# Kernel tuning notes

Hardware: AMD Instinct MI355X
Metric: run time of the kernel (lower is better)

The kernel has to match this reference:

```python
import jax, jax.numpy as jnp
import numpy as np

B, N, IN_F = 8, 1024, 512
H, D = 4, 128  # num_heads, out_features; H*D == IN_F for residual
LN_EPS = 1e-5
NEG_INF = -1e9


def setup_inputs() -> dict:
    key = jax.random.key(0)
    ks = jax.random.split(key, 7)
    x = jax.random.normal(ks[0], (B, N, IN_F), dtype=jnp.float32)
    mask = jax.random.randint(ks[1], (B, N), 0, 2, dtype=jnp.int32)
    # xavier-uniform-ish init scales
    W = jax.random.uniform(ks[2], (IN_F, H * D), dtype=jnp.float32, minval=-1.0, maxval=1.0) * (1.414 * np.sqrt(6.0 / (IN_F + H * D)))
    a_src = jax.random.uniform(ks[3], (H, D), dtype=jnp.float32, minval=-1.0, maxval=1.0) * (1.414 * np.sqrt(6.0 / (H + D)))
    a_dst = jax.random.uniform(ks[4], (H, D), dtype=jnp.float32, minval=-1.0, maxval=1.0) * (1.414 * np.sqrt(6.0 / (H + D)))
    gamma = jnp.ones((H * D,), dtype=jnp.float32)
    beta = jnp.zeros((H * D,), dtype=jnp.float32)
    return {"x": x, "mask": mask, "W": W, "a_src": a_src, "a_dst": a_dst, "gamma": gamma, "beta": beta}


def _layernorm(y, gamma, beta):
    mu = jnp.mean(y, axis=-1, keepdims=True)
    var = jnp.var(y, axis=-1, keepdims=True)
    return (y - mu) * jax.lax.rsqrt(var + LN_EPS) * gamma + beta


def reference(x, mask, W, a_src, a_dst, gamma, beta):
    b, n, _ = x.shape
    h = (x @ W).reshape(b, n, H, D)                      # [B,N,H,D]
    e_i = jnp.einsum('bnhd,hd->bnh', h, a_src)           # [B,N,H]
    e_j = jnp.einsum('bnhd,hd->bnh', h, a_dst)           # [B,N,H]
    e = jax.nn.leaky_relu(e_i[:, :, None, :] + e_j[:, None, :, :], 0.2)  # [B,N,N,H]
    mm = mask[:, None, :, None] * mask[:, :, None, None]  # [B,N,N,1]
    e = jnp.where(mm == 0, NEG_INF, e)
    attn = jax.nn.softmax(e, axis=2)                     # softmax over neighbors j
    h_prime = jnp.einsum('bnjh,bjhd->bnhd', attn, h).reshape(b, n, H * D)
    return _layernorm(h_prime + x, gamma, beta)
```

## Files before the change

kernel.cpp:

```cpp
#include <hip/hip_runtime.h>
#include <math.h>

#define Bsz 8
#define Nn 1024
#define Ff 512
#define Hh 4
#define Dd 128

typedef float f32x4 __attribute__((ext_vector_type(4)));
typedef short bf16x8 __attribute__((ext_vector_type(8)));

__device__ inline uint f2b1(float a) {
    union { float f; uint u; } v; v.f = a;
    return (v.u + 0x7fffu + ((v.u >> 16) & 1u)) >> 16;
}
__device__ inline uint f2b_pk(float a, float b) { return f2b1(a) | (f2b1(b) << 16); }


__global__ __launch_bounds__(256) void conv_xw(const float* __restrict__ X,
                                               const float* __restrict__ Wm,
                                               ushort* __restrict__ Xc,
                                               ushort* __restrict__ Wc) {
    __shared__ float tile[8 * 520];
    const int bi = blockIdx.x, tid = threadIdx.x;
    if (bi < 512) {
        const int mtile = (bi & 7) * 64 + (bi >> 3);
        const int kblk = tid >> 2, m15b = (tid & 3) * 4;
        #pragma unroll
        for (int c = 0; c < 4; ++c) {
            int m15 = m15b + c;
            const float4* xp = (const float4*)(X + (size_t)(mtile * 16 + m15) * Ff + kblk * 8);
            float4 f0 = xp[0], f1 = xp[1];
            uint4 o = { f2b_pk(f0.x, f0.y), f2b_pk(f0.z, f0.w),
                        f2b_pk(f1.x, f1.y), f2b_pk(f1.z, f1.w) };
            *(uint4*)(Xc + (((size_t)(mtile * 64 + kblk) * 16 + m15) << 3)) = o;
        }
    } else {
        const int kb = bi - 512;
        const int l = tid & 63, wv = tid >> 6;
        const int col0 = l * 8;
        #pragma unroll
        for (int rsel = 0; rsel < 2; ++rsel) {
            int kr = wv + rsel * 4;
            const float4* wp = (const float4*)(Wm + (size_t)(kb * 8 + kr) * Ff + col0);
            float4 a = wp[0], c = wp[1];
            *(float4*)(&tile[kr * 520 + col0]) = a;
            *(float4*)(&tile[kr * 520 + col0 + 4]) = c;
        }
        __syncthreads();
        #pragma unroll
        for (int rsel = 0; rsel < 2; ++rsel) {
            int n = tid + rsel * 256;
            float v[8];
            #pragma unroll
            for (int u = 0; u < 8; ++u) v[u] = tile[u * 520 + n];
            uint4 o = { f2b_pk(v[0], v[1]), f2b_pk(v[2], v[3]),
                        f2b_pk(v[4], v[5]), f2b_pk(v[6], v[7]) };
            int nc = n >> 7, nt = (n >> 4) & 7, n15 = n & 15;
            *(uint4*)(Wc + ((size_t)(((nc * 64 + kb) * 8 + nt) * 16 + n15) << 3)) = o;
        }
    }
}

__global__ __launch_bounds__(256, 2) void gemm_xw(const ushort* __restrict__ Xc,
                                                  const ushort* __restrict__ Wc,
                                                  const float* __restrict__ a_src,
                                                  const float* __restrict__ a_dst,
                                                  ushort* __restrict__ hT,
                                                  float* __restrict__ ei,
                                                  float* __restrict__ ej) {
    const int idx = blockIdx.x;
    const int b = idx & 7, sub = idx >> 3;
    const int mi = sub & 15, nc = sub >> 4;
    const int tid = threadIdx.x;
    const int w = tid >> 6, lane = tid & 63, quad = lane >> 4, l16 = lane & 15;
    const int mtile = (b * 16 + mi) * 4 + w;

    f32x4 z = {0.f, 0.f, 0.f, 0.f};
    f32x4 acc[8];
    #pragma unroll
    for (int nt = 0; nt < 8; ++nt) acc[nt] = z;

    const ushort* ap = Xc + ((size_t)mtile << 13) + quad * 128 + l16 * 8;
    const ushort* bp = Wc + ((size_t)nc << 16) + quad * 1024 + l16 * 8;

    bf16x8 ab[2];
    bf16x8 bb[2][8];
    ab[0] = *(const bf16x8*)(ap);
    ab[1] = *(const bf16x8*)(ap + 512);
    #pragma unroll
    for (int nt = 0; nt < 8; ++nt) {
        bb[0][nt] = *(const bf16x8*)(bp + nt * 128);
        bb[1][nt] = *(const bf16x8*)(bp + 4096 + nt * 128);
    }

    #pragma unroll 2
    for (int s = 0; s < 16; ++s) {
        const int c = s & 1;
        #pragma unroll
        for (int nt = 0; nt < 8; ++nt)
            acc[nt] = __builtin_amdgcn_mfma_f32_16x16x32_bf16(ab[c], bb[c][nt], acc[nt], 0, 0, 0);
        if (s + 2 < 16) {
            ab[c] = *(const bf16x8*)(ap + (s + 2) * 512);
            #pragma unroll
            for (int nt = 0; nt < 8; ++nt)
                bb[c][nt] = *(const bf16x8*)(bp + (s + 2) * 4096 + nt * 128);
        }
    }

    const int nseq = (mi * 4 + w) * 16 + quad * 4;
    const int jb = nseq >> 5, js = nseq & 31;
    #pragma unroll
    for (int nt = 0; nt < 8; ++nt) {
        uint2 pv;
        pv.x = f2b_pk(acc[nt][0], acc[nt][1]);
        pv.y = f2b_pk(acc[nt][2], acc[nt][3]);
        int hd = nc * 128 + nt * 16 + l16;
        *(uint2*)(hT + ((size_t)(b * 32 + jb)) * 16384 + (size_t)hd * 32 + js) = pv;
    }

    {
        float as4[8], ad4[8];
        #pragma unroll
        for (int nt = 0; nt < 8; ++nt) {
            as4[nt] = a_src[nc * 128 + nt * 16 + l16];
            ad4[nt] = a_dst[nc * 128 + nt * 16 + l16];
        }
        #pragma unroll
        for (int rr = 0; rr < 4; ++rr) {
            float v1 = 0.f, v2 = 0.f;
            #pragma unroll
            for (int nt = 0; nt < 8; ++nt) {
                v1 += acc[nt][rr] * as4[nt];
                v2 += acc[nt][rr] * ad4[nt];
            }
            #pragma unroll
            for (int off = 1; off < 16; off <<= 1) {
                v1 += __shfl_xor(v1, off);
                v2 += __shfl_xor(v2, off);
            }
            if (l16 == 0) {
                int n = nseq + rr;
                ei[((b * 4 + nc) << 10) + n] = v1;
                ej[((b * 4 + nc) << 10) + n] = v2;
            }
        }
    }
}

__global__ __launch_bounds__(512, 2) void attn_pv(const ushort* __restrict__ hT,
                                                  const float* __restrict__ ei_g,
                                                  const float* __restrict__ ej_g,
                                                  const int* __restrict__ mask,
                                                  const float* __restrict__ X,
                                                  const float* __restrict__ gamma,
                                                  const float* __restrict__ beta,
                                                  float* __restrict__ out) {
    __shared__ float s_ep[32 * 516];
    __shared__ float s_as[4][32];

    const int idx = blockIdx.x;
    const int b = idx & 7, i0 = (idx >> 3) * 32;
    const int tid = threadIdx.x;
    const int w = tid >> 6, w4 = w & 3, jh = w >> 2;
    const int lane = tid & 63, quad = lane >> 4, l16 = lane & 15;

    const float* ejh = ej_g + ((b * 4 + w4) << 10);
    const int* mkb = mask + (b << 10);

    float maxej = -3.0e38f;
    #pragma unroll
    for (int k = 0; k < 16; ++k) maxej = fmaxf(maxej, ejh[lane + 64 * k]);
    #pragma unroll
    for (int off = 1; off < 64; off <<= 1) maxej = fmaxf(maxej, __shfl_xor(maxej, off));

    const float ei0 = ei_g[((b * 4 + w4) << 10) + i0 + l16];
    const float ei1 = ei_g[((b * 4 + w4) << 10) + i0 + 16 + l16];
    const int mi0 = mkb[i0 + l16];
    const int mi1 = mkb[i0 + 16 + l16];
    float m0, m1;
    { float t = ei0 + maxej; m0 = mi0 ? fmaxf(t, 0.2f * t) : -1e9f; }
    { float t = ei1 + maxej; m1 = mi1 ? fmaxf(t, 0.2f * t) : -1e9f; }

    f32x4 z = {0.f, 0.f, 0.f, 0.f};
    f32x4 acc[2][8], asum[2];
    #pragma unroll
    for (int it = 0; it < 2; ++it) { asum[it] = z;
        #pragma unroll
        for (int dt = 0; dt < 8; ++dt) acc[it][dt] = z; }
    bf16x8 ones;
    #pragma unroll
    for (int q = 0; q < 8; ++q) ones[q] = (short)0x3F80;

    const ushort* hTb = hT + ((size_t)(b * 32)) * 16384 + (size_t)(w4 * 128) * 32
                        + l16 * 32 + quad * 8;

    bf16x8 B[2][8];
    #pragma unroll
    for (int c = 0; c < 2; ++c) {
        const ushort* h0 = hTb + (size_t)(jh * 16 + c) * 16384;
        #pragma unroll
        for (int dt = 0; dt < 8; ++dt) B[c][dt] = *(const bf16x8*)(h0 + dt * 512);
    }

    #pragma unroll 2
    for (int r = 0; r < 16; ++r) {
        const int c = r & 1;
        const int jq = (jh * 16 + r) * 32 + quad * 8;
        float4 e0 = *(const float4*)(ejh + jq);
        float4 e1 = *(const float4*)(ejh + jq + 4);
        int4 q0 = *(const int4*)(mkb + jq);
        int4 q1 = *(const int4*)(mkb + jq + 4);
        float ev[8] = {e0.x, e0.y, e0.z, e0.w, e1.x, e1.y, e1.z, e1.w};
        int   mv[8] = {q0.x, q0.y, q0.z, q0.w, q1.x, q1.y, q1.z, q1.w};
        float wv0[8], wv1[8];
        #pragma unroll
        for (int u = 0; u < 8; ++u) {
            float t0 = ei0 + ev[u];
            float l0 = fmaxf(t0, 0.2f * t0);
            wv0[u] = __expf(((mi0 && mv[u]) ? l0 : -1e9f) - m0);
            float t1 = ei1 + ev[u];
            float l1 = fmaxf(t1, 0.2f * t1);
            wv1[u] = __expf(((mi1 && mv[u]) ? l1 : -1e9f) - m1);
        }
        union { uint4 u; bf16x8 v; } af0, af1;
        af0.u.x = f2b_pk(wv0[0], wv0[1]); af0.u.y = f2b_pk(wv0[2], wv0[3]);
        af0.u.z = f2b_pk(wv0[4], wv0[5]); af0.u.w = f2b_pk(wv0[6], wv0[7]);
        af1.u.x = f2b_pk(wv1[0], wv1[1]); af1.u.y = f2b_pk(wv1[2], wv1[3]);
        af1.u.z = f2b_pk(wv1[4], wv1[5]); af1.u.w = f2b_pk(wv1[6], wv1[7]);
        asum[0] = __builtin_amdgcn_mfma_f32_16x16x32_bf16(af0.v, ones, asum[0], 0, 0, 0);
        asum[1] = __builtin_amdgcn_mfma_f32_16x16x32_bf16(af1.v, ones, asum[1], 0, 0, 0);
        #pragma unroll
        for (int dt = 0; dt < 8; ++dt) {
            acc[0][dt] = __builtin_amdgcn_mfma_f32_16x16x32_bf16(af0.v, B[c][dt], acc[0][dt], 0, 0, 0);
            acc[1][dt] = __builtin_amdgcn_mfma_f32_16x16x32_bf16(af1.v, B[c][dt], acc[1][dt], 0, 0, 0);
        }
        if (r + 2 < 16) {
            const ushort* hn = hTb + (size_t)(jh * 16 + r + 2) * 16384;
            #pragma unroll
            for (int dt = 0; dt < 8; ++dt) B[c][dt] = *(const bf16x8*)(hn + dt * 512);
        }
    }

    if (jh == 1) {
        #pragma unroll
        for (int it = 0; it < 2; ++it)
            #pragma unroll
            for (int dt = 0; dt < 8; ++dt)
                #pragma unroll
                for (int rr = 0; rr < 4; ++rr)
                    s_ep[(it * 16 + quad * 4 + rr) * 516 + w4 * 128 + dt * 16 + l16] =
                        acc[it][dt][rr];
        if (l16 == 0) {
            #pragma unroll
            for (int it = 0; it < 2; ++it)
                #pragma unroll
                for (int rr = 0; rr < 4; ++rr)
                    s_as[w4][it * 16 + quad * 4 + rr] = asum[it][rr];
        }
    }
    __syncthreads();
    if (jh == 0) {
        float rs[2][4];
        #pragma unroll
        for (int it = 0; it < 2; ++it)
            #pragma unroll
            for (int rr = 0; rr < 4; ++rr)
                rs[it][rr] = 1.f / (asum[it][rr] + s_as[w4][it * 16 + quad * 4 + rr]);
        #pragma unroll
        for (int it = 0; it < 2; ++it)
            #pragma unroll
            for (int dt = 0; dt < 8; ++dt)
                #pragma unroll
                for (int rr = 0; rr < 4; ++rr) {
                    int off = (it * 16 + quad * 4 + rr) * 516 + w4 * 128 + dt * 16 + l16;
                    s_ep[off] = (acc[it][dt][rr] + s_ep[off]) * rs[it][rr];
                }
    }
    __syncthreads();

    #pragma unroll
    for (int q = 0; q < 4; ++q) {
        int ir = w * 4 + q;
        int ig = i0 + ir;
        float4 p0 = *(const float4*)(&s_ep[ir * 516 + lane * 8]);
        float4 p1 = *(const float4*)(&s_ep[ir * 516 + lane * 8 + 4]);
        const float* xp = X + (((size_t)((b << 10) + ig)) << 9) + lane * 8;
        float4 x0 = *(const float4*)(xp);
        float4 x1 = *(const float4*)(xp + 4);
        float v[8] = {p0.x + x0.x, p0.y + x0.y, p0.z + x0.z, p0.w + x0.w,
                      p1.x + x1.x, p1.y + x1.y, p1.z + x1.z, p1.w + x1.w};
        float s1 = 0.f, s2 = 0.f;
        #pragma unroll
        for (int u = 0; u < 8; ++u) { s1 += v[u]; s2 += v[u] * v[u]; }
        #pragma unroll
        for (int off = 1; off < 64; off <<= 1) { s1 += __shfl_xor(s1, off); s2 += __shfl_xor(s2, off); }
        float mean = s1 * (1.f / 512.f);
        float var  = s2 * (1.f / 512.f) - mean * mean;
        float rstd = rsqrtf(var + 1e-5f);
        int f0i = lane * 8;
        float4 g0 = *(const float4*)(gamma + f0i);
        float4 g1 = *(const float4*)(gamma + f0i + 4);
        float4 be0 = *(const float4*)(beta + f0i);
        float4 be1 = *(const float4*)(beta + f0i + 4);
        float* op = out + (((size_t)((b << 10) + ig)) << 9) + f0i;
        float4 o0, o1;
        o0.x = (v[0] - mean) * rstd * g0.x + be0.x;
        o0.y = (v[1] - mean) * rstd * g0.y + be0.y;
        o0.z = (v[2] - mean) * rstd * g0.z + be0.z;
        o0.w = (v[3] - mean) * rstd * g0.w + be0.w;
        o1.x = (v[4] - mean) * rstd * g1.x + be1.x;
        o1.y = (v[5] - mean) * rstd * g1.y + be1.y;
        o1.z = (v[6] - mean) * rstd * g1.z + be1.z;
        o1.w = (v[7] - mean) * rstd * g1.w + be1.w;
        *(float4*)op = o0;
        *(float4*)(op + 4) = o1;
    }
}

extern "C" void kernel_launch(void* const* d_in, const int* in_sizes, int n_in,
                              void* d_out, int out_size, void* d_ws, size_t ws_size,
                              hipStream_t stream) {
    const float* x     = (const float*)d_in[0];
    const int*   mask  = (const int*)d_in[1];
    const float* W     = (const float*)d_in[2];
    const float* a_src = (const float*)d_in[3];
    const float* a_dst = (const float*)d_in[4];
    const float* gamma = (const float*)d_in[5];
    const float* beta  = (const float*)d_in[6];
    float* out = (float*)d_out;

    ushort* hT = (ushort*)d_ws;
    ushort* Xc = hT + (size_t)8 * 512 * 1024;
    ushort* Wc = Xc + (size_t)8 * 1024 * 512;
    float* ei = (float*)(Wc + (size_t)512 * 512);
    float* ej = ei + 32768;

    conv_xw<<<dim3(576), 256, 0, stream>>>(x, W, Xc, Wc);
    gemm_xw<<<dim3(512), 256, 0, stream>>>(Xc, Wc, a_src, a_dst, hT, ei, ej);
    attn_pv<<<dim3(256), 512, 0, stream>>>(hT, ei, ej, mask, x, gamma, beta, out);
}
```

Before: 126.2 us.

## Fuse X bf16 conversion into GEMM loads and use exp2 with log2e-scaled logits

Removes the separate pass that converted X to a tiled bf16 buffer. The GEMM now reads fp32 X directly and converts it to bf16 in registers, which saves a full write and re-read of X through global memory. The attention logits are pre-scaled by log2(e) so the softmax can call the hardware exp2 instruction instead of __expf. The trade-off is that the GEMM A-operand loads become strided fp32 row reads of twice the size, which may be less coalesced than the old pre-tiled layout.

```diff
diff --git a/kernel.cpp b/kernel.cpp
--- a/kernel.cpp
+++ b/kernel.cpp
@@ -10,6 +10,8 @@
 typedef float f32x4 __attribute__((ext_vector_type(4)));
 typedef short bf16x8 __attribute__((ext_vector_type(8)));
 
+#define LOG2E 1.44269504f
+
 __device__ inline uint f2b1(float a) {
     union { float f; uint u; } v; v.f = a;
     return (v.u + 0x7fffu + ((v.u >> 16) & 1u)) >> 16;
@@ -17,52 +19,35 @@
 __device__ inline uint f2b_pk(float a, float b) { return f2b1(a) | (f2b1(b) << 16); }
 
 
-__global__ __launch_bounds__(256) void conv_xw(const float* __restrict__ X,
-                                               const float* __restrict__ Wm,
-                                               ushort* __restrict__ Xc,
-                                               ushort* __restrict__ Wc) {
+__global__ __launch_bounds__(256) void conv_w(const float* __restrict__ Wm,
+                                              ushort* __restrict__ Wc) {
     __shared__ float tile[8 * 520];
-    const int bi = blockIdx.x, tid = threadIdx.x;
-    if (bi < 512) {
-        const int mtile = (bi & 7) * 64 + (bi >> 3);
-        const int kblk = tid >> 2, m15b = (tid & 3) * 4;
-        #pragma unroll
-        for (int c = 0; c < 4; ++c) {
-            int m15 = m15b + c;
-            const float4* xp = (const float4*)(X + (size_t)(mtile * 16 + m15) * Ff + kblk * 8);
-            float4 f0 = xp[0], f1 = xp[1];
-            uint4 o = { f2b_pk(f0.x, f0.y), f2b_pk(f0.z, f0.w),
-                        f2b_pk(f1.x, f1.y), f2b_pk(f1.z, f1.w) };
-            *(uint4*)(Xc + (((size_t)(mtile * 64 + kblk) * 16 + m15) << 3)) = o;
-        }
-    } else {
-        const int kb = bi - 512;
-        const int l = tid & 63, wv = tid >> 6;
-        const int col0 = l * 8;
-        #pragma unroll
-        for (int rsel = 0; rsel < 2; ++rsel) {
-            int kr = wv + rsel * 4;
-            const float4* wp = (const float4*)(Wm + (size_t)(kb * 8 + kr) * Ff + col0);
-            float4 a = wp[0], c = wp[1];
-            *(float4*)(&tile[kr * 520 + col0]) = a;
-            *(float4*)(&tile[kr * 520 + col0 + 4]) = c;
-        }
-        __syncthreads();
-        #pragma unroll
-        for (int rsel = 0; rsel < 2; ++rsel) {
-            int n = tid + rsel * 256;
-            float v[8];
-            #pragma unroll
-            for (int u = 0; u < 8; ++u) v[u] = tile[u * 520 + n];
-            uint4 o = { f2b_pk(v[0], v[1]), f2b_pk(v[2], v[3]),
-                        f2b_pk(v[4], v[5]), f2b_pk(v[6], v[7]) };
-            int nc = n >> 7, nt = (n >> 4) & 7, n15 = n & 15;
-            *(uint4*)(Wc + ((size_t)(((nc * 64 + kb) * 8 + nt) * 16 + n15) << 3)) = o;
-        }
-    }
-}
-
-__global__ __launch_bounds__(256, 2) void gemm_xw(const ushort* __restrict__ Xc,
+    const int kb = blockIdx.x, tid = threadIdx.x;
+    const int l = tid & 63, wv = tid >> 6;
+    const int col0 = l * 8;
+    #pragma unroll
+    for (int rsel = 0; rsel < 2; ++rsel) {
+        int kr = wv + rsel * 4;
+        const float4* wp = (const float4*)(Wm + (size_t)(kb * 8 + kr) * Ff + col0);
+        float4 a = wp[0], c = wp[1];
+        *(float4*)(&tile[kr * 520 + col0]) = a;
+        *(float4*)(&tile[kr * 520 + col0 + 4]) = c;
+    }
+    __syncthreads();
+    #pragma unroll
+    for (int rsel = 0; rsel < 2; ++rsel) {
+        int n = tid + rsel * 256;
+        float v[8];
+        #pragma unroll
+        for (int u = 0; u < 8; ++u) v[u] = tile[u * 520 + n];
+        uint4 o = { f2b_pk(v[0], v[1]), f2b_pk(v[2], v[3]),
+                    f2b_pk(v[4], v[5]), f2b_pk(v[6], v[7]) };
+        int nc = n >> 7, nt = (n >> 4) & 7, n15 = n & 15;
+        *(uint4*)(Wc + ((size_t)(((nc * 64 + kb) * 8 + nt) * 16 + n15) << 3)) = o;
+    }
+}
+
+__global__ __launch_bounds__(256, 2) void gemm_xw(const float* __restrict__ X,
                                                   const ushort* __restrict__ Wc,
                                                   const float* __restrict__ a_src,
                                                   const float* __restrict__ a_dst,
@@ -81,13 +66,21 @@
     #pragma unroll
     for (int nt = 0; nt < 8; ++nt) acc[nt] = z;
 
-    const ushort* ap = Xc + ((size_t)mtile << 13) + quad * 128 + l16 * 8;
+    const float* ap = X + (size_t)(mtile * 16 + l16) * Ff + quad * 8;
     const ushort* bp = Wc + ((size_t)nc << 16) + quad * 1024 + l16 * 8;
+
+#define LOADA(s, dst) { \
+        float4 f0_ = *(const float4*)(ap + (s) * 32); \
+        float4 f1_ = *(const float4*)(ap + (s) * 32 + 4); \
+        union { uint4 u; bf16x8 v; } o_; \
+        o_.u.x = f2b_pk(f0_.x, f0_.y); o_.u.y = f2b_pk(f0_.z, f0_.w); \
+        o_.u.z = f2b_pk(f1_.x, f1_.y); o_.u.w = f2b_pk(f1_.z, f1_.w); \
+        dst = o_.v; }
 
     bf16x8 ab[2];
     bf16x8 bb[2][8];
-    ab[0] = *(const bf16x8*)(ap);
-    ab[1] = *(const bf16x8*)(ap + 512);
+    LOADA(0, ab[0]);
+    LOADA(1, ab[1]);
     #pragma unroll
     for (int nt = 0; nt < 8; ++nt) {
         bb[0][nt] = *(const bf16x8*)(bp + nt * 128);
@@ -101,12 +94,13 @@
         for (int nt = 0; nt < 8; ++nt)
             acc[nt] = __builtin_amdgcn_mfma_f32_16x16x32_bf16(ab[c], bb[c][nt], acc[nt], 0, 0, 0);
         if (s + 2 < 16) {
-            ab[c] = *(const bf16x8*)(ap + (s + 2) * 512);
+            LOADA(s + 2, ab[c]);
             #pragma unroll
             for (int nt = 0; nt < 8; ++nt)
                 bb[c][nt] = *(const bf16x8*)(bp + (s + 2) * 4096 + nt * 128);
         }
     }
+#undef LOADA
 
     const int nseq = (mi * 4 + w) * 16 + quad * 4;
     const int jb = nseq >> 5, js = nseq & 31;
@@ -123,8 +117,8 @@
         float as4[8], ad4[8];
         #pragma unroll
         for (int nt = 0; nt < 8; ++nt) {
-            as4[nt] = a_src[nc * 128 + nt * 16 + l16];
-            ad4[nt] = a_dst[nc * 128 + nt * 16 + l16];
+            as4[nt] = a_src[nc * 128 + nt * 16 + l16] * LOG2E;
+            ad4[nt] = a_dst[nc * 128 + nt * 16 + l16] * LOG2E;
         }
         #pragma unroll
         for (int rr = 0; rr < 4; ++rr) {
@@ -218,10 +212,10 @@
         for (int u = 0; u < 8; ++u) {
             float t0 = ei0 + ev[u];
             float l0 = fmaxf(t0, 0.2f * t0);
-            wv0[u] = __expf(((mi0 && mv[u]) ? l0 : -1e9f) - m0);
+            wv0[u] = __builtin_amdgcn_exp2f(((mi0 && mv[u]) ? l0 : -1e9f) - m0);
             float t1 = ei1 + ev[u];
             float l1 = fmaxf(t1, 0.2f * t1);
-            wv1[u] = __expf(((mi1 && mv[u]) ? l1 : -1e9f) - m1);
+            wv1[u] = __builtin_amdgcn_exp2f(((mi1 && mv[u]) ? l1 : -1e9f) - m1);
         }
         union { uint4 u; bf16x8 v; } af0, af1;
         af0.u.x = f2b_pk(wv0[0], wv0[1]); af0.u.y = f2b_pk(wv0[2], wv0[3]);
@@ -331,12 +325,11 @@
     float* out = (float*)d_out;
 
     ushort* hT = (ushort*)d_ws;
-    ushort* Xc = hT + (size_t)8 * 512 * 1024;
-    ushort* Wc = Xc + (size_t)8 * 1024 * 512;
+    ushort* Wc = hT + (size_t)8 * 512 * 1024;
     float* ei = (float*)(Wc + (size_t)512 * 512);
     float* ej = ei + 32768;
 
-    conv_xw<<<dim3(576), 256, 0, stream>>>(x, W, Xc, Wc);
-    gemm_xw<<<dim3(512), 256, 0, stream>>>(Xc, Wc, a_src, a_dst, hT, ei, ej);
+    conv_w<<<dim3(64), 256, 0, stream>>>(W, Wc);
+    gemm_xw<<<dim3(512), 256, 0, stream>>>(x, Wc, a_src, a_dst, hT, ei, ej);
     attn_pv<<<dim3(256), 512, 0, stream>>>(hT, ei, ej, mask, x, gamma, beta, out);
 }
```

Result: no change. 125.4 us (-0.6%).
